# Optimization experiments

Measured on AMD Instinct MI355X. Metric: run time of the kernel, lower is better.

The kernel has to match this reference:

```python
import jax, jax.numpy as jnp
import numpy as np

NUM_NEIGHBORS = 10
BN_EPS = 1e-5


def setup_inputs() -> dict:
    key = jax.random.key(0)
    ks = jax.random.split(key, 6)
    B, N, D = 8, 4096, 64
    x = jax.random.normal(ks[0], (B, N, D), jnp.float32)

    def w(k, shape):
        return jax.random.normal(k, shape, jnp.float32) * 0.05

    return {
        "x": x,
        "gamma": jnp.ones((D,), jnp.float32),
        "beta": jnp.zeros((D,), jnp.float32),
        "W1": w(ks[1], (128, 128)), "b1": jnp.zeros((128,), jnp.float32),
        "W2": w(ks[2], (128, 64)), "b2": jnp.zeros((64,), jnp.float32),
        "W3": w(ks[3], (64, 64)), "b3": jnp.zeros((64,), jnp.float32),
        "Wg": w(ks[4], (128, 64)), "bg": jnp.zeros((64,), jnp.float32),
    }


def reference(x, gamma, beta, W1, b1, W2, b2, W3, b3, Wg, bg):
    B, N, D = x.shape
    K = NUM_NEIGHBORS

    # BatchNorm1d in train mode: normalize over all B*N rows with batch stats
    xf = x.reshape(-1, D)
    mu = jnp.mean(xf, axis=0)
    var = jnp.mean((xf - mu) ** 2, axis=0)  # biased, as torch BN uses
    xn = (((xf - mu) / jnp.sqrt(var + BN_EPS)) * gamma + beta).reshape(B, N, D)

    # KNN in feature space (standard DGCNN gather_neighbours)
    sq = jnp.sum(xn * xn, axis=-1)  # [B,N]
    dist = sq[:, :, None] + sq[:, None, :] - 2.0 * jnp.einsum("bnd,bmd->bnm", xn, xn)
    _, idx = jax.lax.top_k(-dist, K)  # [B,N,K] indices of nearest (incl. self)

    # gather neighbor features: neigh[b,n,k,:] = xn[b, idx[b,n,k], :]
    neigh = jax.vmap(lambda f, i: f[i])(xn, idx)  # [B,N,K,D]

    exp = jnp.broadcast_to(xn[:, :, None, :], (B, N, K, D))
    edge = jnp.concatenate([exp, exp - neigh], axis=-1)  # [B,N,K,2D]

    h = jax.nn.relu(edge @ W1 + b1)
    h = jax.nn.relu(h @ W2 + b2)
    h = jax.nn.relu(h @ W3 + b3)  # [B,N,K,64]

    vert = jnp.max(h, axis=2)  # max over neighbors -> [B,N,64]
    g = jnp.max(vert, axis=1, keepdims=True)  # global max-pool [B,1,64]
    cat = jnp.concatenate([vert, jnp.broadcast_to(g, vert.shape)], axis=-1)  # [B,N,128]
    return jax.nn.relu(cat @ Wg + bg)  # [B,N,64]
```

## Files before the change

### kernel.cpp

```cpp
#include <hip/hip_runtime.h>
#include <hip/hip_fp16.h>
#include <float.h>

#define BB 8
#define NN 4096
#define DD 64
#define KNBR 10
#define ROWS (BB*NN)

typedef _Float16 f16x8 __attribute__((ext_vector_type(8)));
typedef float f32x4 __attribute__((ext_vector_type(4)));

__global__ void k_bn_stats(const float* __restrict__ x, float* __restrict__ stats) {
  __shared__ float ls[2][4][64];
  int d = threadIdx.x & 63;
  int g = threadIdx.x >> 6;
  float s = 0.f, s2 = 0.f;
  for (int r = blockIdx.x * 4 + g; r < ROWS; r += gridDim.x * 4) {
    float val = x[r * 64 + d];
    s += val;
    s2 = fmaf(val, val, s2);
  }
  ls[0][g][d] = s;
  ls[1][g][d] = s2;
  __syncthreads();
  if (g == 0) {
    atomicAdd(&stats[d],      ls[0][0][d] + ls[0][1][d] + ls[0][2][d] + ls[0][3][d]);
    atomicAdd(&stats[64 + d], ls[1][0][d] + ls[1][1][d] + ls[1][2][d] + ls[1][3][d]);
  }
}

__global__ void k_bn_finalize(const float* __restrict__ stats,
                              const float* __restrict__ gamma,
                              const float* __restrict__ beta,
                              float* __restrict__ ss) {
  int d = threadIdx.x;
  const float inv = 1.f / 32768.f;
  float mu  = stats[d] * inv;
  float var = stats[64 + d] * inv - mu * mu;
  float sc  = gamma[d] / sqrtf(var + 1e-5f);
  ss[d]      = sc;
  ss[64 + d] = beta[d] - mu * sc;
}

__global__ void k_normalize(const float* __restrict__ x, const float* __restrict__ ss,
                            float* __restrict__ xn, float* __restrict__ sq,
                            _Float16* __restrict__ xh, _Float16* __restrict__ xl) {
  int row = blockIdx.x * 4 + (threadIdx.x >> 6);
  int d = threadIdx.x & 63;
  int idx = row * 64 + d;
  float val = fmaf(x[idx], ss[d], ss[64 + d]);
  xn[idx] = val;
  _Float16 h = (_Float16)val;
  _Float16 l = (_Float16)(val - (float)h);
  xh[idx] = h;
  xl[idx] = l;
  float p = val * val;
  #pragma unroll
  for (int off = 32; off > 0; off >>= 1) p += __shfl_xor(p, off);
  if (d == 0) sq[row] = p;
}

__global__ __launch_bounds__(256, 2) void k_knn(const _Float16* __restrict__ xh,
                                                const _Float16* __restrict__ xl,
                                                const float* __restrict__ sq,
                                                int* __restrict__ knn) {
  __shared__ __align__(16) float lds[16640];
  __shared__ float thrs[64];
  __shared__ int cnts[64];
  const int tid = threadIdx.x;
  const int w = tid >> 6, lane = tid & 63;
  const int l15 = lane & 15, lg = lane >> 4;
  const int b = blockIdx.x >> 6;
  const int rowbase = (blockIdx.x & 63) << 6;
  const int bN = b * NN;
  const _Float16* __restrict__ xhb = xh + (size_t)bN * 64;
  const _Float16* __restrict__ xlb = xl + (size_t)bN * 64;

  char* wbase = (char*)lds + w * 16640;
  char* Bhi = wbase;
  char* Blo = wbase + 4096;
  float* Dw = (float*)(wbase + 8192);

  f16x8 Ah[4][2], Al[4][2];
  #pragma unroll
  for (int mt = 0; mt < 4; ++mt) {
    #pragma unroll
    for (int ks = 0; ks < 2; ++ks) {
      int r = rowbase + mt * 16 + l15;
      Ah[mt][ks] = *(const f16x8*)(xhb + r * 64 + ks * 32 + lg * 8);
      Al[mt][ks] = *(const f16x8*)(xlb + r * 64 + ks * 32 + lg * 8);
    }
  }

  float bd[10];
  #pragma unroll
  for (int i = 0; i < 10; ++i) bd[i] = FLT_MAX;

  int srow[4], scc[4];
  #pragma unroll
  for (int i = 0; i < 4; ++i) { int c = i * 64 + lane; srow[i] = c >> 3; scc[i] = c & 7; }

  f16x8 sh[4], sl[4];
  {
    int mb0 = w * 32;
    #pragma unroll
    for (int i = 0; i < 4; ++i) {
      sh[i] = *(const f16x8*)(xhb + (mb0 + srow[i]) * 64 + scc[i] * 8);
      sl[i] = *(const f16x8*)(xlb + (mb0 + srow[i]) * 64 + scc[i] * 8);
    }
  }

  float* Drow = Dw + lane * 33;

  #pragma unroll 1
  for (int t = 0; t < 32; ++t) {
    const int mb = (t * 4 + w) * 32;
    const int mb2 = (t < 31) ? ((t + 1) * 4 + w) * 32 : mb;
    float sqv0 = sq[bN + mb + l15];
    float sqv1 = sq[bN + mb + 16 + l15];
    #pragma unroll
    for (int i = 0; i < 4; ++i) {
      int off = srow[i] * 128 + 16 * (scc[i] ^ (srow[i] & 7));
      *(f16x8*)(Bhi + off) = sh[i];
      *(f16x8*)(Blo + off) = sl[i];
    }
    #pragma unroll
    for (int i = 0; i < 4; ++i) {
      sh[i] = *(const f16x8*)(xhb + (mb2 + srow[i]) * 64 + scc[i] * 8);
      sl[i] = *(const f16x8*)(xlb + (mb2 + srow[i]) * 64 + scc[i] * 8);
    }
    f16x8 Bh[2][2], Bl[2][2];
    #pragma unroll
    for (int nt = 0; nt < 2; ++nt) {
      #pragma unroll
      for (int ks = 0; ks < 2; ++ks) {
        int rr2 = nt * 16 + l15;
        int off = rr2 * 128 + 16 * ((ks * 4 + lg) ^ (rr2 & 7));
        Bh[nt][ks] = *(const f16x8*)(Bhi + off);
        Bl[nt][ks] = *(const f16x8*)(Blo + off);
      }
    }
    #pragma unroll
    for (int mt = 0; mt < 4; ++mt) {
      f32x4 a0 = {0.f, 0.f, 0.f, 0.f}, a1 = {0.f, 0.f, 0.f, 0.f};
      #pragma unroll
      for (int ks = 0; ks < 2; ++ks) {
        a0 = __builtin_amdgcn_mfma_f32_16x16x32_f16(Ah[mt][ks], Bh[0][ks], a0, 0, 0, 0);
        a1 = __builtin_amdgcn_mfma_f32_16x16x32_f16(Ah[mt][ks], Bh[1][ks], a1, 0, 0, 0);
        a0 = __builtin_amdgcn_mfma_f32_16x16x32_f16(Ah[mt][ks], Bl[0][ks], a0, 0, 0, 0);
        a1 = __builtin_amdgcn_mfma_f32_16x16x32_f16(Ah[mt][ks], Bl[1][ks], a1, 0, 0, 0);
        a0 = __builtin_amdgcn_mfma_f32_16x16x32_f16(Al[mt][ks], Bh[0][ks], a0, 0, 0, 0);
        a1 = __builtin_amdgcn_mfma_f32_16x16x32_f16(Al[mt][ks], Bh[1][ks], a1, 0, 0, 0);
      }
      int rw = mt * 16 + lg * 4;
      #pragma unroll
      for (int r2 = 0; r2 < 4; ++r2) {
        Dw[(rw + r2) * 33 + l15]      = fmaf(-2.f, a0[r2], sqv0);
        Dw[(rw + r2) * 33 + 16 + l15] = fmaf(-2.f, a1[r2], sqv1);
      }
    }
    #pragma unroll 4
    for (int mm = 0; mm < 32; ++mm) {
      float cd = Drow[mm];
      if (cd < bd[9]) {
        float prev = bd[0];
        bd[0] = fminf(cd, bd[0]);
        #pragma unroll
        for (int j = 1; j < 10; ++j) {
          float cur = bd[j];
          bd[j] = fminf(cur, fmaxf(prev, cd));
          prev = cur;
        }
      }
    }
  }

  __syncthreads();
  float* md = lds;
  #pragma unroll
  for (int i = 0; i < 10; ++i) md[(w * 64 + lane) * 10 + i] = bd[i];
  if (tid < 64) cnts[tid] = 0;
  __syncthreads();
  if (tid < 64) {
    float fd[10];
    #pragma unroll
    for (int i = 0; i < 10; ++i) fd[i] = FLT_MAX;
    for (int w2 = 0; w2 < 4; ++w2) {
      #pragma unroll
      for (int kk = 0; kk < 10; ++kk) {
        float cd = md[(w2 * 64 + tid) * 10 + kk];
        if (cd < fd[9]) {
          float prev = fd[0];
          fd[0] = fminf(cd, fd[0]);
          #pragma unroll
          for (int j = 1; j < 10; ++j) {
            float cur = fd[j];
            fd[j] = fminf(cur, fmaxf(prev, cd));
            prev = cur;
          }
        }
      }
    }
    thrs[tid] = fd[9];
  }
  __syncthreads();

  float thv[4][4];
  #pragma unroll
  for (int mt = 0; mt < 4; ++mt)
    #pragma unroll
    for (int r2 = 0; r2 < 4; ++r2)
      thv[mt][r2] = thrs[mt * 16 + lg * 4 + r2];

  int* knnrow = knn + (size_t)(bN + rowbase) * KNBR;

  {
    int mb0 = w * 32;
    #pragma unroll
    for (int i = 0; i < 4; ++i) {
      sh[i] = *(const f16x8*)(xhb + (mb0 + srow[i]) * 64 + scc[i] * 8);
      sl[i] = *(const f16x8*)(xlb + (mb0 + srow[i]) * 64 + scc[i] * 8);
    }
  }
  #pragma unroll 1
  for (int t = 0; t < 32; ++t) {
    const int mb = (t * 4 + w) * 32;
    const int mb2 = (t < 31) ? ((t + 1) * 4 + w) * 32 : mb;
    float sqv0 = sq[bN + mb + l15];
    float sqv1 = sq[bN + mb + 16 + l15];
    #pragma unroll
    for (int i = 0; i < 4; ++i) {
      int off = srow[i] * 128 + 16 * (scc[i] ^ (srow[i] & 7));
      *(f16x8*)(Bhi + off) = sh[i];
      *(f16x8*)(Blo + off) = sl[i];
    }
    #pragma unroll
    for (int i = 0; i < 4; ++i) {
      sh[i] = *(const f16x8*)(xhb + (mb2 + srow[i]) * 64 + scc[i] * 8);
      sl[i] = *(const f16x8*)(xlb + (mb2 + srow[i]) * 64 + scc[i] * 8);
    }
    f16x8 Bh[2][2], Bl[2][2];
    #pragma unroll
    for (int nt = 0; nt < 2; ++nt) {
      #pragma unroll
      for (int ks = 0; ks < 2; ++ks) {
        int rr2 = nt * 16 + l15;
        int off = rr2 * 128 + 16 * ((ks * 4 + lg) ^ (rr2 & 7));
        Bh[nt][ks] = *(const f16x8*)(Bhi + off);
        Bl[nt][ks] = *(const f16x8*)(Blo + off);
      }
    }
    #pragma unroll
    for (int mt = 0; mt < 4; ++mt) {
      f32x4 a0 = {0.f, 0.f, 0.f, 0.f}, a1 = {0.f, 0.f, 0.f, 0.f};
      #pragma unroll
      for (int ks = 0; ks < 2; ++ks) {
        a0 = __builtin_amdgcn_mfma_f32_16x16x32_f16(Ah[mt][ks], Bh[0][ks], a0, 0, 0, 0);
        a1 = __builtin_amdgcn_mfma_f32_16x16x32_f16(Ah[mt][ks], Bh[1][ks], a1, 0, 0, 0);
        a0 = __builtin_amdgcn_mfma_f32_16x16x32_f16(Ah[mt][ks], Bl[0][ks], a0, 0, 0, 0);
        a1 = __builtin_amdgcn_mfma_f32_16x16x32_f16(Ah[mt][ks], Bl[1][ks], a1, 0, 0, 0);
        a0 = __builtin_amdgcn_mfma_f32_16x16x32_f16(Al[mt][ks], Bh[0][ks], a0, 0, 0, 0);
        a1 = __builtin_amdgcn_mfma_f32_16x16x32_f16(Al[mt][ks], Bh[1][ks], a1, 0, 0, 0);
      }
      #pragma unroll
      for (int r2 = 0; r2 < 4; ++r2) {
        float d0 = fmaf(-2.f, a0[r2], sqv0);
        float d1 = fmaf(-2.f, a1[r2], sqv1);
        int row = mt * 16 + lg * 4 + r2;
        if (d0 <= thv[mt][r2]) {
          int slot = atomicAdd(&cnts[row], 1);
          if (slot < KNBR) knnrow[row * KNBR + slot] = bN + mb + l15;
        }
        if (d1 <= thv[mt][r2]) {
          int slot = atomicAdd(&cnts[row], 1);
          if (slot < KNBR) knnrow[row * KNBR + slot] = bN + mb + 16 + l15;
        }
      }
    }
  }
}

__global__ void k_uv(const float* __restrict__ xn, const float* __restrict__ W1,
                     const float* __restrict__ b1, float* __restrict__ u,
                     float* __restrict__ v) {
  __shared__ float xs[64 * 64];
  const int tid = threadIdx.x;
  const int o = tid & 127;
  const bool isU = tid < 128;
  const int rowbase = blockIdx.x * 64;

  float wreg[64];
  #pragma unroll
  for (int d = 0; d < 64; ++d) {
    float bw = W1[(64 + d) * 128 + o];
    wreg[d] = isU ? (W1[d * 128 + o] + bw) : bw;
  }
  const float bb = isU ? b1[o] : 0.f;
  float* __restrict__ dst = isU ? u : v;

  {
    const float4* s4 = (const float4*)(xn + rowbase * 64);
    float4* d4 = (float4*)xs;
    #pragma unroll
    for (int i = 0; i < 4; ++i) d4[tid + 256 * i] = s4[tid + 256 * i];
  }
  __syncthreads();

  for (int r = 0; r < 64; ++r) {
    const float4* xr = (const float4*)(xs + r * 64);
    float a0 = bb, a1 = 0.f, a2 = 0.f, a3 = 0.f;
    #pragma unroll
    for (int q = 0; q < 16; ++q) {
      float4 xv = xr[q];
      a0 = fmaf(xv.x, wreg[4 * q + 0], a0);
      a1 = fmaf(xv.y, wreg[4 * q + 1], a1);
      a2 = fmaf(xv.z, wreg[4 * q + 2], a2);
      a3 = fmaf(xv.w, wreg[4 * q + 3], a3);
    }
    dst[(rowbase + r) * 128 + o] = (a0 + a1) + (a2 + a3);
  }
}

__global__ __launch_bounds__(256, 2) void k_edge(const float* __restrict__ uu,
                                                 const float* __restrict__ vv,
                                                 const int* __restrict__ knn,
                                                 const float* __restrict__ W2,
                                                 const float* __restrict__ b2,
                                                 const float* __restrict__ W3,
                                                 const float* __restrict__ b3,
                                                 float* __restrict__ vert) {
  __shared__ __align__(16) _Float16 W3Ts[64 * 72];
  __shared__ __align__(16) _Float16 h2buf[4][16 * 88];
  __shared__ int vmaxs[4][512];
  const int tid = threadIdx.x;
  const int w = tid >> 6, lane = tid & 63;
  const int l15 = lane & 15, lg = lane >> 4;

  for (int i = tid; i < 64 * 64; i += 256) {
    int o3 = i >> 6, k2 = i & 63;
    W3Ts[o3 * 72 + k2] = (_Float16)W3[k2 * 64 + o3];
  }
  f16x8 w2f[4][4];
  #pragma unroll
  for (int ks = 0; ks < 4; ++ks) {
    #pragma unroll
    for (int nt = 0; nt < 4; ++nt) {
      f16x8 t;
      #pragma unroll
      for (int j = 0; j < 8; ++j)
        t[j] = (_Float16)W2[(ks * 32 + lg * 8 + j) * 64 + nt * 16 + l15];
      w2f[ks][nt] = t;
    }
  }
  float bias2[4], bias3[4];
  #pragma unroll
  for (int nt = 0; nt < 4; ++nt) { bias2[nt] = b2[nt * 16 + l15]; bias3[nt] = b3[nt * 16 + l15]; }

  _Float16* h2w = h2buf[w];
  int* vmaxw = vmaxs[w];
  #pragma unroll
  for (int q = 0; q < 8; ++q) vmaxw[lane * 8 + q] = 0;
  __syncthreads();

  const int g = blockIdx.x * 4 + w;
  const int n0 = g * 8;
  const int ebase = n0 * KNBR;
  #pragma unroll 1
  for (int mt = 0; mt < 5; ++mt) {
    const int e = mt * 16 + l15;
    const int m = knn[ebase + e];
    const int n = n0 + e / 10;
    const float* Up = uu + (size_t)n * 128 + lg * 8;
    const float* Vp = vv + (size_t)m * 128 + lg * 8;
    f16x8 A[4];
    #pragma unroll
    for (int ks = 0; ks < 4; ++ks) {
      float4 ua = *(const float4*)(Up + ks * 32);
      float4 ub = *(const float4*)(Up + ks * 32 + 4);
      float4 va = *(const float4*)(Vp + ks * 32);
      float4 vb = *(const float4*)(Vp + ks * 32 + 4);
      f16x8 t;
      t[0] = (_Float16)fmaxf(ua.x - va.x, 0.f);
      t[1] = (_Float16)fmaxf(ua.y - va.y, 0.f);
      t[2] = (_Float16)fmaxf(ua.z - va.z, 0.f);
      t[3] = (_Float16)fmaxf(ua.w - va.w, 0.f);
      t[4] = (_Float16)fmaxf(ub.x - vb.x, 0.f);
      t[5] = (_Float16)fmaxf(ub.y - vb.y, 0.f);
      t[6] = (_Float16)fmaxf(ub.z - vb.z, 0.f);
      t[7] = (_Float16)fmaxf(ub.w - vb.w, 0.f);
      A[ks] = t;
    }
    f32x4 acc[4];
    #pragma unroll
    for (int nt = 0; nt < 4; ++nt) { float bbv = bias2[nt]; acc[nt] = (f32x4){bbv, bbv, bbv, bbv}; }
    #pragma unroll
    for (int ks = 0; ks < 4; ++ks) {
      #pragma unroll
      for (int nt = 0; nt < 4; ++nt)
        acc[nt] = __builtin_amdgcn_mfma_f32_16x16x32_f16(A[ks], w2f[ks][nt], acc[nt], 0, 0, 0);
    }
    #pragma unroll
    for (int nt = 0; nt < 4; ++nt) {
      #pragma unroll
      for (int r = 0; r < 4; ++r)
        h2w[(lg * 4 + r) * 88 + nt * 16 + l15] = (_Float16)fmaxf(acc[nt][r], 0.f);
    }
    f16x8 A3[2];
    #pragma unroll
    for (int ks2 = 0; ks2 < 2; ++ks2)
      A3[ks2] = *(const f16x8*)(h2w + l15 * 88 + ks2 * 32 + lg * 8);
    f32x4 c3[4];
    #pragma unroll
    for (int nt = 0; nt < 4; ++nt) { float bbv = bias3[nt]; c3[nt] = (f32x4){bbv, bbv, bbv, bbv}; }
    #pragma unroll
    for (int ks2 = 0; ks2 < 2; ++ks2) {
      #pragma unroll
      for (int nt = 0; nt < 4; ++nt) {
        f16x8 bf = *(const f16x8*)(W3Ts + (nt * 16 + l15) * 72 + ks2 * 32 + lg * 8);
        c3[nt] = __builtin_amdgcn_mfma_f32_16x16x32_f16(A3[ks2], bf, c3[nt], 0, 0, 0);
      }
    }
    #pragma unroll
    for (int nt = 0; nt < 4; ++nt) {
      #pragma unroll
      for (int r = 0; r < 4; ++r) {
        float val = fmaxf(c3[nt][r], 0.f);
        int e2 = mt * 16 + lg * 4 + r;
        int p = e2 / 10;
        atomicMax(&vmaxw[p * 64 + nt * 16 + l15], __float_as_int(val));
      }
    }
  }
  {
    int p2 = lane >> 3, c0 = (lane & 7) * 8;
    const int* vp = &vmaxw[p2 * 64 + c0];
    float4 r0, r1;
    r0.x = __int_as_float(vp[0]); r0.y = __int_as_float(vp[1]);
    r0.z = __int_as_float(vp[2]); r0.w = __int_as_float(vp[3]);
    r1.x = __int_as_float(vp[4]); r1.y = __int_as_float(vp[5]);
    r1.z = __int_as_float(vp[6]); r1.w = __int_as_float(vp[7]);
    *(float4*)(vert + (size_t)(n0 + p2) * 64 + c0) = r0;
    *(float4*)(vert + (size_t)(n0 + p2) * 64 + c0 + 4) = r1;
  }
}

__global__ void k_gmax(const float* __restrict__ vert, float* __restrict__ g) {
  __shared__ float red[4][64];
  int b = blockIdx.x >> 4, chunk = blockIdx.x & 15;
  int sub = threadIdx.x >> 6, o = threadIdx.x & 63;
  float vm = 0.f;
  for (int j = 0; j < 64; ++j) {
    int r = chunk * 256 + j * 4 + sub;
    vm = fmaxf(vm, vert[(b * NN + r) * 64 + o]);
  }
  red[sub][o] = vm;
  __syncthreads();
  if (sub == 0) {
    float mm = fmaxf(fmaxf(red[0][o], red[1][o]), fmaxf(red[2][o], red[3][o]));
    atomicMax((int*)&g[b * 64 + o], __float_as_int(mm));
  }
}

__global__ void k_gb(const float* __restrict__ g, const float* __restrict__ Wg,
                     const float* __restrict__ bg, float* __restrict__ gb) {
  int t = threadIdx.x;
  int b = t >> 6, o = t & 63;
  float acc = bg[o];
  #pragma unroll
  for (int i = 0; i < 64; ++i)
    acc = fmaf(g[b * 64 + i], Wg[(64 + i) * 64 + o], acc);
  gb[b * 64 + o] = acc;
}

__global__ void k_final(const float* __restrict__ vert, const float* __restrict__ Wg,
                        const float* __restrict__ gb, float* __restrict__ out) {
  __shared__ float Wgs[64 * 64];
  int tid = threadIdx.x, w = tid >> 6, lane = tid & 63;
  for (int i = tid; i < 4096; i += 256) Wgs[i] = Wg[i];
  __syncthreads();
  int gw = blockIdx.x * 4 + w;
  for (int j = 0; j < 4; ++j) {
    int n = gw + 8192 * j;
    int b = n >> 12;
    float vrow = vert[n * 64 + lane];
    float ac0 = gb[b * 64 + lane], ac1 = 0.f, ac2 = 0.f, ac3 = 0.f;
    #pragma unroll
    for (int i = 0; i < 64; i += 4) {
      ac0 = fmaf(__shfl(vrow, i),     Wgs[i * 64 + lane],       ac0);
      ac1 = fmaf(__shfl(vrow, i + 1), Wgs[(i + 1) * 64 + lane], ac1);
      ac2 = fmaf(__shfl(vrow, i + 2), Wgs[(i + 2) * 64 + lane], ac2);
      ac3 = fmaf(__shfl(vrow, i + 3), Wgs[(i + 3) * 64 + lane], ac3);
    }
    out[n * 64 + lane] = fmaxf((ac0 + ac1) + (ac2 + ac3), 0.f);
  }
}

extern "C" void kernel_launch(void* const* d_in, const int* in_sizes, int n_in,
                              void* d_out, int out_size, void* d_ws, size_t ws_size,
                              hipStream_t stream) {
  const float* x     = (const float*)d_in[0];
  const float* gamma = (const float*)d_in[1];
  const float* beta  = (const float*)d_in[2];
  const float* W1    = (const float*)d_in[3];
  const float* b1    = (const float*)d_in[4];
  const float* W2    = (const float*)d_in[5];
  const float* b2    = (const float*)d_in[6];
  const float* W3    = (const float*)d_in[7];
  const float* b3    = (const float*)d_in[8];
  const float* Wg    = (const float*)d_in[9];
  const float* bg    = (const float*)d_in[10];
  float* out = (float*)d_out;

  float* ws    = (float*)d_ws;
  float* stats = ws;
  float* ss    = ws + 128;
  float* xn    = ws + 256;
  float* sq    = xn + 2097152;
  int*   knn   = (int*)(sq + 32768);
  float* u     = (float*)(knn + 327680);
  float* v     = u + 4194304;
  float* vert  = v + 4194304;
  float* g     = vert + 2097152;
  float* gb    = g + 512;
  _Float16* xh = (_Float16*)(gb + 512);
  _Float16* xl = (_Float16*)(gb + 512 + 1048576);

  hipMemsetAsync(stats, 0, 128 * sizeof(float), stream);
  hipMemsetAsync(g, 0, 512 * sizeof(float), stream);

  k_bn_stats<<<256, 256, 0, stream>>>(x, stats);
  k_bn_finalize<<<1, 64, 0, stream>>>(stats, gamma, beta, ss);
  k_normalize<<<8192, 256, 0, stream>>>(x, ss, xn, sq, xh, xl);
  k_knn<<<512, 256, 0, stream>>>(xh, xl, sq, knn);
  k_uv<<<512, 256, 0, stream>>>(xn, W1, b1, u, v);
  k_edge<<<1024, 256, 0, stream>>>(u, v, knn, W2, b2, W3, b3, vert);
  k_gmax<<<128, 256, 0, stream>>>(vert, g);
  k_gb<<<1, 512, 0, stream>>>(g, Wg, bg, gb);
  k_final<<<2048, 256, 0, stream>>>(vert, Wg, gb, out);
}
```

Baseline: 469.3 us.

## Halve KNN rows per block and split candidate scan across lane halves

Each KNN block now handles 32 query rows instead of 64, doubling the grid to 1024 blocks. Two lanes share each row, each scanning half of the 32 candidate columns per tile, and their top-10 lists are merged with a cross-half shuffle. The goal is more parallelism and a shorter serial insertion-sort loop per lane. In exchange, each block does less MFMA work per B-tile load, so global and LDS traffic for the candidate tiles doubles, and there is extra merge work. The final merge loop also exits early once a sorted candidate cannot enter the list.

```diff
diff --git a/kernel.cpp b/kernel.cpp
--- a/kernel.cpp
+++ b/kernel.cpp
@@ -65,26 +65,26 @@
                                                 const _Float16* __restrict__ xl,
                                                 const float* __restrict__ sq,
                                                 int* __restrict__ knn) {
-  __shared__ __align__(16) float lds[16640];
-  __shared__ float thrs[64];
-  __shared__ int cnts[64];
+  __shared__ __align__(16) char lds[49664];
+  __shared__ float thrs[32];
+  __shared__ int cnts[32];
   const int tid = threadIdx.x;
   const int w = tid >> 6, lane = tid & 63;
   const int l15 = lane & 15, lg = lane >> 4;
-  const int b = blockIdx.x >> 6;
-  const int rowbase = (blockIdx.x & 63) << 6;
+  const int b = blockIdx.x >> 7;
+  const int rowbase = (blockIdx.x & 127) << 5;
   const int bN = b * NN;
   const _Float16* __restrict__ xhb = xh + (size_t)bN * 64;
   const _Float16* __restrict__ xlb = xl + (size_t)bN * 64;
 
-  char* wbase = (char*)lds + w * 16640;
+  char* wbase = lds + w * 12416;
   char* Bhi = wbase;
   char* Blo = wbase + 4096;
   float* Dw = (float*)(wbase + 8192);
 
-  f16x8 Ah[4][2], Al[4][2];
-  #pragma unroll
-  for (int mt = 0; mt < 4; ++mt) {
+  f16x8 Ah[2][2], Al[2][2];
+  #pragma unroll
+  for (int mt = 0; mt < 2; ++mt) {
     #pragma unroll
     for (int ks = 0; ks < 2; ++ks) {
       int r = rowbase + mt * 16 + l15;
@@ -111,7 +111,8 @@
     }
   }
 
-  float* Drow = Dw + lane * 33;
+  const int rr = lane & 31, hh = lane >> 5;
+  float* Drow = Dw + rr * 33 + hh * 16;
 
   #pragma unroll 1
   for (int t = 0; t < 32; ++t) {
@@ -142,7 +143,7 @@
       }
     }
     #pragma unroll
-    for (int mt = 0; mt < 4; ++mt) {
+    for (int mt = 0; mt < 2; ++mt) {
       f32x4 a0 = {0.f, 0.f, 0.f, 0.f}, a1 = {0.f, 0.f, 0.f, 0.f};
       #pragma unroll
       for (int ks = 0; ks < 2; ++ks) {
@@ -161,7 +162,7 @@
       }
     }
     #pragma unroll 4
-    for (int mm = 0; mm < 32; ++mm) {
+    for (int mm = 0; mm < 16; ++mm) {
       float cd = Drow[mm];
       if (cd < bd[9]) {
         float prev = bd[0];
@@ -176,20 +177,42 @@
     }
   }
 
-  __syncthreads();
-  float* md = lds;
-  #pragma unroll
-  for (int i = 0; i < 10; ++i) md[(w * 64 + lane) * 10 + i] = bd[i];
-  if (tid < 64) cnts[tid] = 0;
-  __syncthreads();
-  if (tid < 64) {
+  {
+    float ov[10];
+    #pragma unroll
+    for (int i = 0; i < 10; ++i) ov[i] = __shfl_xor(bd[i], 32);
+    #pragma unroll
+    for (int i = 0; i < 10; ++i) {
+      float cd = ov[i];
+      if (cd < bd[9]) {
+        float prev = bd[0];
+        bd[0] = fminf(cd, bd[0]);
+        #pragma unroll
+        for (int j = 1; j < 10; ++j) {
+          float cur = bd[j];
+          bd[j] = fminf(cur, fmaxf(prev, cd));
+          prev = cur;
+        }
+      }
+    }
+  }
+
+  __syncthreads();
+  float* md = (float*)lds;
+  if (lane < 32) {
+    #pragma unroll
+    for (int i = 0; i < 10; ++i) md[(w * 32 + rr) * 10 + i] = bd[i];
+  }
+  if (tid < 32) cnts[tid] = 0;
+  __syncthreads();
+  if (tid < 32) {
     float fd[10];
     #pragma unroll
     for (int i = 0; i < 10; ++i) fd[i] = FLT_MAX;
     for (int w2 = 0; w2 < 4; ++w2) {
-      #pragma unroll
+      #pragma unroll 1
       for (int kk = 0; kk < 10; ++kk) {
-        float cd = md[(w2 * 64 + tid) * 10 + kk];
+        float cd = md[(w2 * 32 + tid) * 10 + kk];
         if (cd < fd[9]) {
           float prev = fd[0];
           fd[0] = fminf(cd, fd[0]);
@@ -199,16 +222,16 @@
             fd[j] = fminf(cur, fmaxf(prev, cd));
             prev = cur;
           }
-        }
+        } else break;
       }
     }
     thrs[tid] = fd[9];
   }
   __syncthreads();
 
-  float thv[4][4];
-  #pragma unroll
-  for (int mt = 0; mt < 4; ++mt)
+  float thv[2][4];
+  #pragma unroll
+  for (int mt = 0; mt < 2; ++mt)
     #pragma unroll
     for (int r2 = 0; r2 < 4; ++r2)
       thv[mt][r2] = thrs[mt * 16 + lg * 4 + r2];
@@ -252,7 +275,7 @@
       }
     }
     #pragma unroll
-    for (int mt = 0; mt < 4; ++mt) {
+    for (int mt = 0; mt < 2; ++mt) {
       f32x4 a0 = {0.f, 0.f, 0.f, 0.f}, a1 = {0.f, 0.f, 0.f, 0.f};
       #pragma unroll
       for (int ks = 0; ks < 2; ++ks) {
@@ -532,7 +555,7 @@
   k_bn_stats<<<256, 256, 0, stream>>>(x, stats);
   k_bn_finalize<<<1, 64, 0, stream>>>(stats, gamma, beta, ss);
   k_normalize<<<8192, 256, 0, stream>>>(x, ss, xn, sq, xh, xl);
-  k_knn<<<512, 256, 0, stream>>>(xh, xl, sq, knn);
+  k_knn<<<1024, 256, 0, stream>>>(xh, xl, sq, knn);
   k_uv<<<512, 256, 0, stream>>>(xn, W1, b1, u, v);
   k_edge<<<1024, 256, 0, stream>>>(u, v, knn, W2, b2, W3, b3, vert);
   k_gmax<<<128, 256, 0, stream>>>(vert, g);
```

Measured after the change: 492.9 us. 5.0% more time.
